# Kernel tuning notes

Measured on AMD Instinct MI355X. Metric: run time of the kernel, lower is better.

## Reference

```python
import jax, jax.numpy as jnp
import numpy as np

N = 200_000      # n_reflns
NIMG = 500       # n_images
DMETA = 24       # metadata features
WIDTH = 32       # mlp_width
HID = 64         # hidden_units = 2*width (FeedForward default)
DEPTH = 20       # mlp_depth
NPOST = 2        # Normal posterior: (loc, scale)
EPS = 1e-12
KLW = 0.01       # scaling_kl_weight


def setup_inputs() -> dict:
    key = jax.random.key(0)
    ks = jax.random.split(key, 10)
    metadata = jax.random.normal(ks[0], (N, DMETA), jnp.float32)
    iobs = jax.random.normal(ks[1], (N, 1), jnp.float32)
    sigiobs = jax.random.uniform(ks[2], (N, 1), jnp.float32)
    image_ids = jnp.sort(jax.random.randint(ks[3], (N,), 0, NIMG)).astype(jnp.int32)
    n_reflns_per_image = jnp.bincount(image_ids, length=NIMG).astype(jnp.int32)
    d_img = DMETA + 2  # concat(metadata, iobs, sigiobs)
    w_img_in = jax.random.normal(ks[4], (d_img, WIDTH), jnp.float32) / np.float32(np.sqrt(d_img))
    b_img_in = jnp.zeros((WIDTH,), jnp.float32)
    w_scale_in = jax.random.normal(ks[5], (DMETA, WIDTH), jnp.float32) / np.float32(np.sqrt(DMETA))
    b_scale_in = jnp.zeros((WIDTH,), jnp.float32)
    # shared residual FeedForward stack (share_weights=True): x + W2 @ relu(W1 @ x)
    mlp_w1 = jax.random.normal(ks[6], (DEPTH, WIDTH, HID), jnp.float32) / np.float32(np.sqrt(WIDTH))
    mlp_b1 = jnp.zeros((DEPTH, HID), jnp.float32)
    mlp_w2 = jax.random.normal(ks[7], (DEPTH, HID, WIDTH), jnp.float32) * np.float32(0.1 / np.sqrt(HID))
    mlp_b2 = jnp.zeros((DEPTH, WIDTH), jnp.float32)
    w_out = jax.random.normal(ks[8], (WIDTH, NPOST), jnp.float32) / np.float32(np.sqrt(WIDTH))
    b_out = jnp.zeros((NPOST,), jnp.float32)
    return {
        'metadata': metadata, 'iobs': iobs, 'sigiobs': sigiobs,
        'w_img_in': w_img_in, 'b_img_in': b_img_in,
        'w_scale_in': w_scale_in, 'b_scale_in': b_scale_in,
        'mlp_w1': mlp_w1, 'mlp_b1': mlp_b1, 'mlp_w2': mlp_w2, 'mlp_b2': mlp_b2,
        'w_out': w_out, 'b_out': b_out,
        'image_ids_in_this_batch': image_ids,
        'n_reflns_per_image': n_reflns_per_image,
        'mc_samples': 32,
    }


def _mlp(h, w1, b1, w2, b2):
    # depth residual FF blocks, weights stacked along leading DEPTH axis
    def block(h, ws):
        wa, ba, wb, bb = ws
        h = h + (jax.nn.relu(h @ wa + ba) @ wb + bb)
        return h, None
    h, _ = jax.lax.scan(block, h, (w1, b1, w2, b2))
    return h


def reference(metadata, iobs, sigiobs,
              w_img_in, b_img_in, w_scale_in, b_scale_in,
              mlp_w1, mlp_b1, mlp_w2, mlp_b2, w_out, b_out,
              image_ids_in_this_batch, n_reflns_per_image, mc_samples):
    image = jnp.concatenate([metadata, iobs, sigiobs], axis=-1)   # (N, DMETA+2)
    h = image @ w_img_in + b_img_in                               # (N, W)
    h = _mlp(h, mlp_w1, mlp_b1, mlp_w2, mlp_b2)
    nimg = n_reflns_per_image.shape[0]
    sums = jax.ops.segment_sum(h, image_ids_in_this_batch, num_segments=nimg)
    counts = jnp.maximum(n_reflns_per_image, 1).astype(h.dtype)[:, None]
    pooled = sums / counts                                        # (NIMG, W) image-average pool
    s = metadata @ w_scale_in + b_scale_in + pooled[image_ids_in_this_batch]
    s = _mlp(s, mlp_w1, mlp_b1, mlp_w2, mlp_b2)                   # shared weights
    params = s @ w_out + b_out                                    # (N, 2)
    loc = params[:, 0]
    scale = jax.nn.softplus(params[:, 1]) + EPS
    # rsample from Normal(loc, scale), mc_samples draws
    noise = jax.random.normal(jax.random.key(42), (mc_samples, loc.shape[0]), loc.dtype)
    z = loc + scale * noise                                       # (S, N)
    # MC KL estimate: mean_s[log q(z) - log p(z)], p = Laplace(0, 1)
    log_q = -0.5 * jnp.square(noise) - jnp.log(scale) - np.float32(0.5 * np.log(2.0 * np.pi))
    log_p = -jnp.abs(z) - np.float32(np.log(2.0))
    kl_div = KLW * jnp.mean(log_q - log_p, axis=0)                # (N,)
    return z.T, kl_div
```

## Files before the change

### kernel.cpp

```cpp
#include <hip/hip_runtime.h>
#include <stdint.h>

#define N_ROWS 200000
#define NIMG   500
#define DMETA  24
#define WIDTH  32
#define HID    64
#define DEPTH  20
#define MC     32
#define NSTR   18

typedef __attribute__((ext_vector_type(8))) short bf16x8;
typedef __attribute__((ext_vector_type(4))) float f32x4;

#define MFMA(a, b, acc) __builtin_amdgcn_mfma_f32_16x16x32_bf16((a), (b), (acc), 0, 0, 0)

#define OFF_W1H  64000
#define OFF_W1L  145920
#define OFF_W2H  227840
#define OFF_W2L  309760
#define OFF_WIH  391680
#define OFF_WIL  393728
#define OFF_WSH  395776
#define OFF_WSL  397824

__device__ __forceinline__ uint32_t rotl32(uint32_t x, int r) {
    return (x << r) | (x >> (32 - r));
}

__device__ __forceinline__ uint32_t tf_bits(uint32_t j) {
    const uint32_t ks1 = 42u, ks2 = 0x1BD11BDAu ^ 42u;
    uint32_t x0 = 0u, x1 = j + ks1;
#define R4(a,b,c,d) \
    x0 += x1; x1 = rotl32(x1,(a)); x1 ^= x0; \
    x0 += x1; x1 = rotl32(x1,(b)); x1 ^= x0; \
    x0 += x1; x1 = rotl32(x1,(c)); x1 ^= x0; \
    x0 += x1; x1 = rotl32(x1,(d)); x1 ^= x0;
    R4(13,15,26,6)  x0 += ks1; x1 += ks2 + 1u;
    R4(17,29,16,24) x0 += ks2; x1 += 0u + 2u;
    R4(13,15,26,6)                x1 += ks1 + 3u;
    R4(17,29,16,24) x0 += ks1; x1 += ks2 + 4u;
    R4(13,15,26,6)  x0 += ks2; x1 += 0u + 5u;
#undef R4
    return x0 ^ x1;
}

__device__ __forceinline__ float bits_to_normal(uint32_t b) {
    float f = __uint_as_float((b >> 9) | 0x3f800000u) - 1.0f;
    const float lo = -0.99999994f;
    float u = fmaxf(lo, f * 2.0f + lo);
    return 1.41421356f * erfinvf(u);
}

__device__ __forceinline__ void split1(float x, short& hi, short& lo) {
    uint32_t b = __float_as_uint(x);
    uint32_t a = b + 0x8000u;
    hi = (short)(a >> 16);
    float r = x - __uint_as_float(a & 0xFFFF0000u);
    lo = (short)(__float_as_uint(r) >> 16);
}

__device__ __forceinline__ void split8p(const float* x, bf16x8& hi, bf16x8& lo) {
    uint32_t hu[4], lu[4];
#pragma unroll
    for (int p = 0; p < 4; ++p) {
        uint32_t b0 = __float_as_uint(x[2 * p]);
        uint32_t b1 = __float_as_uint(x[2 * p + 1]);
        uint32_t a0 = b0 + 0x8000u, a1 = b1 + 0x8000u;
        hu[p] = __builtin_amdgcn_perm(a1, a0, 0x07060302u);
        float r0 = x[2 * p] - __uint_as_float(a0 & 0xFFFF0000u);
        float r1 = x[2 * p + 1] - __uint_as_float(a1 & 0xFFFF0000u);
        lu[p] = __builtin_amdgcn_perm(__float_as_uint(r1), __float_as_uint(r0), 0x07060302u);
    }
    __builtin_memcpy(&hi, hu, 16);
    __builtin_memcpy(&lo, lu, 16);
}

__device__ __forceinline__ void mlp20_x2(
    float* hC0, float* hC1, float* smw0, float* smw1,
    const short* __restrict__ w1fh, const short* __restrict__ w1fl,
    const short* __restrict__ w2fh, const short* __restrict__ w2fl,
    const float* __restrict__ b1, const float* __restrict__ b2,
    int lane, int q, int c) {
    float2* sm20 = (float2*)smw0;
    float2* sm21 = (float2*)smw1;
#pragma unroll 1
    for (int l = 0; l < DEPTH; ++l) {
#pragma unroll
        for (int t = 0; t < 2; ++t) {
            int bi = (16 * t + c) * 9 + 2 * q;
            sm20[bi]     = make_float2(hC0[t * 4 + 0], hC0[t * 4 + 1]);
            sm20[bi + 1] = make_float2(hC0[t * 4 + 2], hC0[t * 4 + 3]);
            sm21[bi]     = make_float2(hC1[t * 4 + 0], hC1[t * 4 + 1]);
            sm21[bi + 1] = make_float2(hC1[t * 4 + 2], hC1[t * 4 + 3]);
        }
        float a0[8], a1[8];
#pragma unroll
        for (int j = 0; j < 8; ++j) a0[j] = smw0[(q * 8 + j) * NSTR + c];
#pragma unroll
        for (int j = 0; j < 8; ++j) a1[j] = smw1[(q * 8 + j) * NSTR + c];
        bf16x8 ah0, al0, ah1, al1;
        split8p(a0, ah0, al0);
        split8p(a1, ah1, al1);
        float C1v0[16], C1v1[16];
#pragma unroll
        for (int t = 0; t < 4; ++t) {
            const int fi = (((l * 4 + t) << 9) + (lane << 3));
            bf16x8 bh = *(const bf16x8*)(w1fh + fi);
            bf16x8 bl = *(const bf16x8*)(w1fl + fi);
            float bb = b1[l * 64 + 16 * t + c];
            f32x4 acc = {0.f, 0.f, 0.f, 0.f};
            acc = MFMA(ah0, bh, acc); acc = MFMA(ah0, bl, acc); acc = MFMA(al0, bh, acc);
            f32x4 acd = {0.f, 0.f, 0.f, 0.f};
            acd = MFMA(ah1, bh, acd); acd = MFMA(ah1, bl, acd); acd = MFMA(al1, bh, acd);
#pragma unroll
            for (int r = 0; r < 4; ++r) {
                C1v0[t * 4 + r] = fmaxf(acc[r] + bb, 0.0f);
                C1v1[t * 4 + r] = fmaxf(acd[r] + bb, 0.0f);
            }
        }
#pragma unroll
        for (int t = 0; t < 4; ++t) {
            int bi = (16 * t + c) * 9 + 2 * q;
            sm20[bi]     = make_float2(C1v0[t * 4 + 0], C1v0[t * 4 + 1]);
            sm20[bi + 1] = make_float2(C1v0[t * 4 + 2], C1v0[t * 4 + 3]);
            sm21[bi]     = make_float2(C1v1[t * 4 + 0], C1v1[t * 4 + 1]);
            sm21[bi + 1] = make_float2(C1v1[t * 4 + 2], C1v1[t * 4 + 3]);
        }
        f32x4 acc0[2], acc1[2];
#pragma unroll
        for (int t2 = 0; t2 < 2; ++t2)
#pragma unroll
            for (int r = 0; r < 4; ++r) {
                acc0[t2][r] = hC0[t2 * 4 + r];
                acc1[t2][r] = hC1[t2 * 4 + r];
            }
#pragma unroll
        for (int kf = 0; kf < 2; ++kf) {
            float e0[8], e1[8];
#pragma unroll
            for (int j = 0; j < 8; ++j) e0[j] = smw0[(kf * 32 + q * 8 + j) * NSTR + c];
#pragma unroll
            for (int j = 0; j < 8; ++j) e1[j] = smw1[(kf * 32 + q * 8 + j) * NSTR + c];
            bf16x8 xh0, xl0, xh1, xl1;
            split8p(e0, xh0, xl0);
            split8p(e1, xh1, xl1);
#pragma unroll
            for (int t2 = 0; t2 < 2; ++t2) {
                const int fi = ((((l * 2 + kf) * 2 + t2) << 9) + (lane << 3));
                bf16x8 bh = *(const bf16x8*)(w2fh + fi);
                bf16x8 bl = *(const bf16x8*)(w2fl + fi);
                acc0[t2] = MFMA(xh0, bh, acc0[t2]);
                acc0[t2] = MFMA(xh0, bl, acc0[t2]);
                acc0[t2] = MFMA(xl0, bh, acc0[t2]);
                acc1[t2] = MFMA(xh1, bh, acc1[t2]);
                acc1[t2] = MFMA(xh1, bl, acc1[t2]);
                acc1[t2] = MFMA(xl1, bh, acc1[t2]);
            }
        }
#pragma unroll
        for (int t2 = 0; t2 < 2; ++t2) {
            float bb = b2[l * 32 + 16 * t2 + c];
#pragma unroll
            for (int r = 0; r < 4; ++r) {
                hC0[t2 * 4 + r] = acc0[t2][r] + bb;
                hC1[t2 * 4 + r] = acc1[t2][r] + bb;
            }
        }
    }
}

__device__ __forceinline__ void input_proj(
    const bf16x8& ah, const bf16x8& al, const short* __restrict__ wfh,
    const short* __restrict__ wfl, const float* __restrict__ bias,
    float* hC, int lane, int c) {
#pragma unroll
    for (int t = 0; t < 2; ++t) {
        bf16x8 bh = *(const bf16x8*)(wfh + ((t << 9) + (lane << 3)));
        bf16x8 bl = *(const bf16x8*)(wfl + ((t << 9) + (lane << 3)));
        f32x4 acc = {0.f, 0.f, 0.f, 0.f};
        acc = MFMA(ah, bh, acc); acc = MFMA(ah, bl, acc); acc = MFMA(al, bh, acc);
        float bb = bias[16 * t + c];
#pragma unroll
        for (int r = 0; r < 4; ++r) hC[t * 4 + r] = acc[r] + bb;
    }
}

__global__ __launch_bounds__(256) void prep_kernel(
    const float* __restrict__ w1, const float* __restrict__ w2,
    const float* __restrict__ wimg, const float* __restrict__ wsc,
    char* __restrict__ wsb) {
    int t = blockIdx.x * 256 + threadIdx.x;
    float* sums = (float*)wsb;
    if (t < 16000) { sums[t] = 0.0f; return; }
    t -= 16000;
    if (t < 40960) {
        int l = t >> 11, r = t & 2047, tt = r >> 9, r2 = r & 511;
        int lane = r2 >> 3, j = r2 & 7;
        int k = (lane >> 4) * 8 + j, n = 16 * tt + (lane & 15);
        short h, lo;
        split1(w1[l * 2048 + k * 64 + n], h, lo);
        ((short*)(wsb + OFF_W1H))[t] = h;
        ((short*)(wsb + OFF_W1L))[t] = lo;
        return;
    }
    t -= 40960;
    if (t < 40960) {
        int l = t >> 11, r = t & 2047, kf = r >> 10, r2 = r & 1023;
        int t2 = r2 >> 9, r3 = r2 & 511, lane = r3 >> 3, j = r3 & 7;
        int k = kf * 32 + (lane >> 4) * 8 + j, n = 16 * t2 + (lane & 15);
        short h, lo;
        split1(w2[l * 2048 + k * 32 + n], h, lo);
        ((short*)(wsb + OFF_W2H))[t] = h;
        ((short*)(wsb + OFF_W2L))[t] = lo;
        return;
    }
    t -= 40960;
    if (t < 1024) {
        int tt = t >> 9, r = t & 511, lane = r >> 3, j = r & 7;
        int k = (lane >> 4) * 8 + j, n = 16 * tt + (lane & 15);
        float v = (k < 26) ? wimg[k * 32 + n] : 0.0f;
        short h, lo;
        split1(v, h, lo);
        ((short*)(wsb + OFF_WIH))[t] = h;
        ((short*)(wsb + OFF_WIL))[t] = lo;
        return;
    }
    t -= 1024;
    if (t < 1024) {
        int tt = t >> 9, r = t & 511, lane = r >> 3, j = r & 7;
        int k = (lane >> 4) * 8 + j, n = 16 * tt + (lane & 15);
        float v = (k < 24) ? wsc[k * 32 + n] : 0.0f;
        short h, lo;
        split1(v, h, lo);
        ((short*)(wsb + OFF_WSH))[t] = h;
        ((short*)(wsb + OFF_WSL))[t] = lo;
        return;
    }
}

__device__ __forceinline__ void load_xfrag(
    const float* __restrict__ md, const float* __restrict__ iobs,
    const float* __restrict__ sig, int base, int q, int c,
    bf16x8& ah, bf16x8& al) {
    float xa[8];
    if (q < 3) {
        const f32x4* rp = (const f32x4*)(md + (size_t)(base + c) * DMETA + q * 8);
        f32x4 v0 = rp[0], v1 = rp[1];
#pragma unroll
        for (int j = 0; j < 4; ++j) { xa[j] = v0[j]; xa[4 + j] = v1[j]; }
    } else {
        xa[0] = iobs ? iobs[base + c] : 0.0f;
        xa[1] = sig ? sig[base + c] : 0.0f;
#pragma unroll
        for (int j = 2; j < 8; ++j) xa[j] = 0.0f;
    }
    split8p(xa, ah, al);
}

__global__ __launch_bounds__(128, 4) void pass_a(
    const float* __restrict__ md, const float* __restrict__ iobs,
    const float* __restrict__ sig, const float* __restrict__ bimg,
    const char* __restrict__ wsb, const float* __restrict__ b1,
    const float* __restrict__ b2, const int* __restrict__ ids,
    float* __restrict__ sums) {
    __shared__ float smat[2][2][64 * NSTR];
    int lane = threadIdx.x & 63, w = threadIdx.x >> 6;
    int q = lane >> 4, c = lane & 15;
    int i0 = (blockIdx.x * 2 + w) * 32;
    float* smw0 = &smat[w][0][0];
    float* smw1 = &smat[w][1][0];

    bf16x8 ah0, al0, ah1, al1;
    load_xfrag(md, iobs, sig, i0, q, c, ah0, al0);
    load_xfrag(md, iobs, sig, i0 + 16, q, c, ah1, al1);

    float hC0[8], hC1[8];
    input_proj(ah0, al0, (const short*)(wsb + OFF_WIH), (const short*)(wsb + OFF_WIL),
               bimg, hC0, lane, c);
    input_proj(ah1, al1, (const short*)(wsb + OFF_WIH), (const short*)(wsb + OFF_WIL),
               bimg, hC1, lane, c);

    mlp20_x2(hC0, hC1, smw0, smw1,
             (const short*)(wsb + OFF_W1H), (const short*)(wsb + OFF_W1L),
             (const short*)(wsb + OFF_W2H), (const short*)(wsb + OFF_W2L),
             b1, b2, lane, q, c);

#pragma unroll
    for (int tile = 0; tile < 2; ++tile) {
        const float* hC = tile ? hC1 : hC0;
        int tb = i0 + tile * 16;
        bool uni = (ids[tb] == ids[tb + 15]);
        if (uni) {
            int id = ids[tb];
#pragma unroll
            for (int t = 0; t < 2; ++t) {
                float s = (hC[t * 4 + 0] + hC[t * 4 + 1]) + (hC[t * 4 + 2] + hC[t * 4 + 3]);
                s += __shfl_xor(s, 16, 64);
                s += __shfl_xor(s, 32, 64);
                if (q == 0) atomicAdd(&sums[id * 32 + 16 * t + c], s);
            }
        } else {
            int idv[4];
#pragma unroll
            for (int r = 0; r < 4; ++r) idv[r] = ids[tb + q * 4 + r];
#pragma unroll
            for (int t = 0; t < 2; ++t)
#pragma unroll
                for (int r = 0; r < 4; ++r)
                    atomicAdd(&sums[idv[r] * 32 + 16 * t + c], hC[t * 4 + r]);
        }
    }
}

__global__ __launch_bounds__(256) void normalize_kernel(float* __restrict__ sums,
                                                        const int* __restrict__ cnts) {
    int t = blockIdx.x * 256 + threadIdx.x;
    if (t < NIMG * WIDTH) {
        int img = t >> 5;
        float cc = (float)max(cnts[img], 1);
        sums[t] = sums[t] / cc;
    }
}

__global__ __launch_bounds__(128, 4) void pass_b(
    const float* __restrict__ md, const float* __restrict__ bsc,
    const char* __restrict__ wsb, const float* __restrict__ b1,
    const float* __restrict__ b2, const float* __restrict__ wout,
    const float* __restrict__ bout, const int* __restrict__ ids,
    const float* __restrict__ pooled, float* __restrict__ out) {
    __shared__ float smat[2][2][64 * NSTR];
    __shared__ float sls[2][64];
    int lane = threadIdx.x & 63, w = threadIdx.x >> 6;
    int q = lane >> 4, c = lane & 15;
    int i0 = (blockIdx.x * 2 + w) * 32;
    float* smw0 = &smat[w][0][0];
    float* smw1 = &smat[w][1][0];

    bf16x8 ah0, al0, ah1, al1;
    load_xfrag(md, nullptr, nullptr, i0, q, c, ah0, al0);
    load_xfrag(md, nullptr, nullptr, i0 + 16, q, c, ah1, al1);

    float hC0[8], hC1[8];
    input_proj(ah0, al0, (const short*)(wsb + OFF_WSH), (const short*)(wsb + OFF_WSL),
               bsc, hC0, lane, c);
    input_proj(ah1, al1, (const short*)(wsb + OFF_WSH), (const short*)(wsb + OFF_WSL),
               bsc, hC1, lane, c);
#pragma unroll
    for (int tile = 0; tile < 2; ++tile) {
        float* hC = tile ? hC1 : hC0;
        int tb = i0 + tile * 16;
        int idv[4];
#pragma unroll
        for (int r = 0; r < 4; ++r) idv[r] = ids[tb + q * 4 + r];
#pragma unroll
        for (int t = 0; t < 2; ++t)
#pragma unroll
            for (int r = 0; r < 4; ++r)
                hC[t * 4 + r] += pooled[idv[r] * 32 + 16 * t + c];
    }

    mlp20_x2(hC0, hC1, smw0, smw1,
             (const short*)(wsb + OFF_W1H), (const short*)(wsb + OFF_W1L),
             (const short*)(wsb + OFF_W2H), (const short*)(wsb + OFF_W2L),
             b1, b2, lane, q, c);

    float wo0[2], wo1[2];
#pragma unroll
    for (int t = 0; t < 2; ++t) {
        float2 wv = ((const float2*)wout)[16 * t + c];
        wo0[t] = wv.x; wo1[t] = wv.y;
    }
#pragma unroll
    for (int tile = 0; tile < 2; ++tile) {
        const float* hC = tile ? hC1 : hC0;
        float p0r[4], p1r[4];
#pragma unroll
        for (int r = 0; r < 4; ++r) {
            p0r[r] = hC[r] * wo0[0] + hC[4 + r] * wo0[1];
            p1r[r] = hC[r] * wo1[0] + hC[4 + r] * wo1[1];
        }
#pragma unroll
        for (int m = 1; m < 16; m <<= 1) {
#pragma unroll
            for (int r = 0; r < 4; ++r) {
                p0r[r] += __shfl_xor(p0r[r], m, 64);
                p1r[r] += __shfl_xor(p1r[r], m, 64);
            }
        }
        if (c == 0) {
#pragma unroll
            for (int r = 0; r < 4; ++r) {
                float loc = p0r[r] + bout[0];
                float pb = p1r[r] + bout[1];
                float scale = fmaxf(pb, 0.0f) + log1pf(expf(-fabsf(pb))) + 1e-12f;
                sls[w][tile * 16 + q * 4 + r] = loc;
                sls[w][32 + tile * 16 + q * 4 + r] = scale;
            }
        }
    }

    int ro = lane & 31, half = lane >> 5;
    int row = i0 + ro;
    float L = sls[w][ro];
    float S = sls[w][32 + ro];
    float lsg = logf(S);
    float kp = 0.0f;
    float* zrow = out + (size_t)row * MC + half * 16;
#pragma unroll 4
    for (int s4 = 0; s4 < 4; ++s4) {
        f32x4 zv;
#pragma unroll
        for (int jj = 0; jj < 4; ++jj) {
            int t = half * 16 + s4 * 4 + jj;
            uint32_t j = (uint32_t)(t * N_ROWS) + (uint32_t)row;
            float n = bits_to_normal(tf_bits(j));
            float z = fmaf(S, n, L);
            zv[jj] = z;
            kp += fmaf(-0.5f, n * n, fabsf(z));
        }
        *(f32x4*)(zrow + s4 * 4) = zv;
    }
    kp += __shfl_xor(kp, 32, 64);
    if (half == 0) {
        out[(size_t)N_ROWS * MC + row] =
            0.01f * (kp * (1.0f / 32.0f) - lsg - 0.91893853320467274f + 0.69314718055994531f);
    }
}

extern "C" void kernel_launch(void* const* d_in, const int* in_sizes, int n_in,
                              void* d_out, int out_size, void* d_ws, size_t ws_size,
                              hipStream_t stream) {
    const float* md   = (const float*)d_in[0];
    const float* iobs = (const float*)d_in[1];
    const float* sig  = (const float*)d_in[2];
    const float* wimg = (const float*)d_in[3];
    const float* bimg = (const float*)d_in[4];
    const float* wsc  = (const float*)d_in[5];
    const float* bsc  = (const float*)d_in[6];
    const float* w1   = (const float*)d_in[7];
    const float* b1   = (const float*)d_in[8];
    const float* w2   = (const float*)d_in[9];
    const float* b2   = (const float*)d_in[10];
    const float* wout = (const float*)d_in[11];
    const float* bout = (const float*)d_in[12];
    const int* ids    = (const int*)d_in[13];
    const int* cnts   = (const int*)d_in[14];
    float* out = (float*)d_out;
    char* wsb = (char*)d_ws;
    float* sums = (float*)wsb;

    const int nblk = N_ROWS / 64;
    prep_kernel<<<391, 256, 0, stream>>>(w1, w2, wimg, wsc, wsb);
    pass_a<<<nblk, 128, 0, stream>>>(md, iobs, sig, bimg, wsb, b1, b2, ids, sums);
    normalize_kernel<<<(NIMG * WIDTH + 255) / 256, 256, 0, stream>>>(sums, cnts);
    pass_b<<<nblk, 128, 0, stream>>>(md, bsc, wsb, b1, b2, wout, bout, ids, sums, out);
}
```

Baseline: 395.4 us.

## Keep MLP activations in registers via transposed 16x16x16 MFMA layout

Rewrites the residual MLP so that weights become the A operand and activations the B operand of 16x16x16 bf16 MFMAs. The output layout of one layer then matches the input layout of the next, so the shared-memory round trip and the LDS re-read that transposed activations each layer are removed. Weight hi/lo fragments are interleaved into one 16-byte load per fragment. Pooling atomics, the pooled gather and the output head are adapted to the new row-per-column layout. The trade-off is twice as many smaller MFMA instructions and different register pressure.

```diff
diff --git a/kernel.cpp b/kernel.cpp
--- a/kernel.cpp
+++ b/kernel.cpp
@@ -8,21 +8,19 @@
 #define HID    64
 #define DEPTH  20
 #define MC     32
-#define NSTR   18
-
+
+typedef __attribute__((ext_vector_type(4))) short bf16x4;
 typedef __attribute__((ext_vector_type(8))) short bf16x8;
 typedef __attribute__((ext_vector_type(4))) float f32x4;
 
-#define MFMA(a, b, acc) __builtin_amdgcn_mfma_f32_16x16x32_bf16((a), (b), (acc), 0, 0, 0)
-
-#define OFF_W1H  64000
-#define OFF_W1L  145920
-#define OFF_W2H  227840
-#define OFF_W2L  309760
-#define OFF_WIH  391680
-#define OFF_WIL  393728
-#define OFF_WSH  395776
-#define OFF_WSL  397824
+__device__ __forceinline__ f32x4 MFMA16(bf16x4 a, bf16x4 b, f32x4 c) {
+    return __builtin_amdgcn_mfma_f32_16x16x16bf16_1k(a, b, c, 0, 0, 0);
+}
+
+#define OFF_W1 64000
+#define OFF_W2 227840
+#define OFF_WI 391680
+#define OFF_WS 395776
 
 __device__ __forceinline__ uint32_t rotl32(uint32_t x, int r) {
     return (x << r) | (x >> (32 - r));
@@ -64,9 +62,8 @@
     uint32_t hu[4], lu[4];
 #pragma unroll
     for (int p = 0; p < 4; ++p) {
-        uint32_t b0 = __float_as_uint(x[2 * p]);
-        uint32_t b1 = __float_as_uint(x[2 * p + 1]);
-        uint32_t a0 = b0 + 0x8000u, a1 = b1 + 0x8000u;
+        uint32_t a0 = __float_as_uint(x[2 * p]) + 0x8000u;
+        uint32_t a1 = __float_as_uint(x[2 * p + 1]) + 0x8000u;
         hu[p] = __builtin_amdgcn_perm(a1, a0, 0x07060302u);
         float r0 = x[2 * p] - __uint_as_float(a0 & 0xFFFF0000u);
         float r1 = x[2 * p + 1] - __uint_as_float(a1 & 0xFFFF0000u);
@@ -76,113 +73,131 @@
     __builtin_memcpy(&lo, lu, 16);
 }
 
-__device__ __forceinline__ void mlp20_x2(
-    float* hC0, float* hC1, float* smw0, float* smw1,
-    const short* __restrict__ w1fh, const short* __restrict__ w1fl,
-    const short* __restrict__ w2fh, const short* __restrict__ w2fl,
+__device__ __forceinline__ void split4p(const float* x, bf16x4& hi, bf16x4& lo) {
+    uint32_t hu[2], lu[2];
+#pragma unroll
+    for (int p = 0; p < 2; ++p) {
+        uint32_t a0 = __float_as_uint(x[2 * p]) + 0x8000u;
+        uint32_t a1 = __float_as_uint(x[2 * p + 1]) + 0x8000u;
+        hu[p] = __builtin_amdgcn_perm(a1, a0, 0x07060302u);
+        float r0 = x[2 * p] - __uint_as_float(a0 & 0xFFFF0000u);
+        float r1 = x[2 * p + 1] - __uint_as_float(a1 & 0xFFFF0000u);
+        lu[p] = __builtin_amdgcn_perm(__float_as_uint(r1), __float_as_uint(r0), 0x07060302u);
+    }
+    __builtin_memcpy(&hi, hu, 8);
+    __builtin_memcpy(&lo, lu, 8);
+}
+
+__device__ __forceinline__ bf16x4 vlo(bf16x8 v) { bf16x4 r = {v[0], v[1], v[2], v[3]}; return r; }
+__device__ __forceinline__ bf16x4 vhi(bf16x8 v) { bf16x4 r = {v[4], v[5], v[6], v[7]}; return r; }
+
+__device__ __forceinline__ void mlp20_reg(
+    float* hC0, float* hC1,
+    const short* __restrict__ w1f, const short* __restrict__ w2f,
     const float* __restrict__ b1, const float* __restrict__ b2,
-    int lane, int q, int c) {
-    float2* sm20 = (float2*)smw0;
-    float2* sm21 = (float2*)smw1;
+    int lane, int q) {
+    const int fo = lane * 8;
 #pragma unroll 1
     for (int l = 0; l < DEPTH; ++l) {
-#pragma unroll
-        for (int t = 0; t < 2; ++t) {
-            int bi = (16 * t + c) * 9 + 2 * q;
-            sm20[bi]     = make_float2(hC0[t * 4 + 0], hC0[t * 4 + 1]);
-            sm20[bi + 1] = make_float2(hC0[t * 4 + 2], hC0[t * 4 + 3]);
-            sm21[bi]     = make_float2(hC1[t * 4 + 0], hC1[t * 4 + 1]);
-            sm21[bi + 1] = make_float2(hC1[t * 4 + 2], hC1[t * 4 + 3]);
-        }
-        float a0[8], a1[8];
-#pragma unroll
-        for (int j = 0; j < 8; ++j) a0[j] = smw0[(q * 8 + j) * NSTR + c];
-#pragma unroll
-        for (int j = 0; j < 8; ++j) a1[j] = smw1[(q * 8 + j) * NSTR + c];
-        bf16x8 ah0, al0, ah1, al1;
-        split8p(a0, ah0, al0);
-        split8p(a1, ah1, al1);
-        float C1v0[16], C1v1[16];
-#pragma unroll
-        for (int t = 0; t < 4; ++t) {
-            const int fi = (((l * 4 + t) << 9) + (lane << 3));
-            bf16x8 bh = *(const bf16x8*)(w1fh + fi);
-            bf16x8 bl = *(const bf16x8*)(w1fl + fi);
-            float bb = b1[l * 64 + 16 * t + c];
-            f32x4 acc = {0.f, 0.f, 0.f, 0.f};
-            acc = MFMA(ah0, bh, acc); acc = MFMA(ah0, bl, acc); acc = MFMA(al0, bh, acc);
-            f32x4 acd = {0.f, 0.f, 0.f, 0.f};
-            acd = MFMA(ah1, bh, acd); acd = MFMA(ah1, bl, acd); acd = MFMA(al1, bh, acd);
+        bf16x8 s0h, s0l, s1h, s1l;
+        split8p(hC0, s0h, s0l);
+        split8p(hC1, s1h, s1l);
+        bf16x4 c0h[2] = {vlo(s0h), vhi(s0h)}, c0l[2] = {vlo(s0l), vhi(s0l)};
+        bf16x4 c1h[2] = {vlo(s1h), vhi(s1h)}, c1l[2] = {vlo(s1l), vhi(s1l)};
+        float Y0[16], Y1[16];
+        const short* wp1 = w1f + l * 4096;
+#pragma unroll
+        for (int Mt = 0; Mt < 4; ++Mt) {
+            f32x4 bb = *(const f32x4*)(b1 + l * 64 + 16 * Mt + 4 * q);
+            f32x4 a0 = {0.f, 0.f, 0.f, 0.f}, a1 = {0.f, 0.f, 0.f, 0.f};
+#pragma unroll
+            for (int Kc = 0; Kc < 2; ++Kc) {
+                bf16x8 wf = *(const bf16x8*)(wp1 + (Mt * 2 + Kc) * 512 + fo);
+                bf16x4 wh = vlo(wf), wl = vhi(wf);
+                a0 = MFMA16(wh, c0h[Kc], a0);
+                a0 = MFMA16(wh, c0l[Kc], a0);
+                a0 = MFMA16(wl, c0h[Kc], a0);
+                a1 = MFMA16(wh, c1h[Kc], a1);
+                a1 = MFMA16(wh, c1l[Kc], a1);
+                a1 = MFMA16(wl, c1h[Kc], a1);
+            }
 #pragma unroll
             for (int r = 0; r < 4; ++r) {
-                C1v0[t * 4 + r] = fmaxf(acc[r] + bb, 0.0f);
-                C1v1[t * 4 + r] = fmaxf(acd[r] + bb, 0.0f);
+                Y0[Mt * 4 + r] = fmaxf(a0[r] + bb[r], 0.0f);
+                Y1[Mt * 4 + r] = fmaxf(a1[r] + bb[r], 0.0f);
             }
         }
-#pragma unroll
-        for (int t = 0; t < 4; ++t) {
-            int bi = (16 * t + c) * 9 + 2 * q;
-            sm20[bi]     = make_float2(C1v0[t * 4 + 0], C1v0[t * 4 + 1]);
-            sm20[bi + 1] = make_float2(C1v0[t * 4 + 2], C1v0[t * 4 + 3]);
-            sm21[bi]     = make_float2(C1v1[t * 4 + 0], C1v1[t * 4 + 1]);
-            sm21[bi + 1] = make_float2(C1v1[t * 4 + 2], C1v1[t * 4 + 3]);
-        }
-        f32x4 acc0[2], acc1[2];
-#pragma unroll
-        for (int t2 = 0; t2 < 2; ++t2)
+        bf16x8 y0h0, y0l0, y0h1, y0l1, y1h0, y1l0, y1h1, y1l1;
+        split8p(Y0, y0h0, y0l0); split8p(Y0 + 8, y0h1, y0l1);
+        split8p(Y1, y1h0, y1l0); split8p(Y1 + 8, y1h1, y1l1);
+        bf16x4 yb0[4] = {vlo(y0h0), vhi(y0h0), vlo(y0h1), vhi(y0h1)};
+        bf16x4 ys0[4] = {vlo(y0l0), vhi(y0l0), vlo(y0l1), vhi(y0l1)};
+        bf16x4 yb1[4] = {vlo(y1h0), vhi(y1h0), vlo(y1h1), vhi(y1h1)};
+        bf16x4 ys1[4] = {vlo(y1l0), vhi(y1l0), vlo(y1l1), vhi(y1l1)};
+        const short* wp2 = w2f + l * 4096;
+#pragma unroll
+        for (int Mt2 = 0; Mt2 < 2; ++Mt2) {
+            f32x4 bb = *(const f32x4*)(b2 + l * 32 + 16 * Mt2 + 4 * q);
+            f32x4 a0, a1;
+#pragma unroll
+            for (int r = 0; r < 4; ++r) { a0[r] = hC0[Mt2 * 4 + r]; a1[r] = hC1[Mt2 * 4 + r]; }
+#pragma unroll
+            for (int Kc = 0; Kc < 4; ++Kc) {
+                bf16x8 wf = *(const bf16x8*)(wp2 + (Mt2 * 4 + Kc) * 512 + fo);
+                bf16x4 wh = vlo(wf), wl = vhi(wf);
+                a0 = MFMA16(wh, yb0[Kc], a0);
+                a0 = MFMA16(wh, ys0[Kc], a0);
+                a0 = MFMA16(wl, yb0[Kc], a0);
+                a1 = MFMA16(wh, yb1[Kc], a1);
+                a1 = MFMA16(wh, ys1[Kc], a1);
+                a1 = MFMA16(wl, yb1[Kc], a1);
+            }
 #pragma unroll
             for (int r = 0; r < 4; ++r) {
-                acc0[t2][r] = hC0[t2 * 4 + r];
-                acc1[t2][r] = hC1[t2 * 4 + r];
+                hC0[Mt2 * 4 + r] = a0[r] + bb[r];
+                hC1[Mt2 * 4 + r] = a1[r] + bb[r];
             }
-#pragma unroll
-        for (int kf = 0; kf < 2; ++kf) {
-            float e0[8], e1[8];
-#pragma unroll
-            for (int j = 0; j < 8; ++j) e0[j] = smw0[(kf * 32 + q * 8 + j) * NSTR + c];
-#pragma unroll
-            for (int j = 0; j < 8; ++j) e1[j] = smw1[(kf * 32 + q * 8 + j) * NSTR + c];
-            bf16x8 xh0, xl0, xh1, xl1;
-            split8p(e0, xh0, xl0);
-            split8p(e1, xh1, xl1);
-#pragma unroll
-            for (int t2 = 0; t2 < 2; ++t2) {
-                const int fi = ((((l * 2 + kf) * 2 + t2) << 9) + (lane << 3));
-                bf16x8 bh = *(const bf16x8*)(w2fh + fi);
-                bf16x8 bl = *(const bf16x8*)(w2fl + fi);
-                acc0[t2] = MFMA(xh0, bh, acc0[t2]);
-                acc0[t2] = MFMA(xh0, bl, acc0[t2]);
-                acc0[t2] = MFMA(xl0, bh, acc0[t2]);
-                acc1[t2] = MFMA(xh1, bh, acc1[t2]);
-                acc1[t2] = MFMA(xh1, bl, acc1[t2]);
-                acc1[t2] = MFMA(xl1, bh, acc1[t2]);
-            }
-        }
-#pragma unroll
-        for (int t2 = 0; t2 < 2; ++t2) {
-            float bb = b2[l * 32 + 16 * t2 + c];
-#pragma unroll
-            for (int r = 0; r < 4; ++r) {
-                hC0[t2 * 4 + r] = acc0[t2][r] + bb;
-                hC1[t2 * 4 + r] = acc1[t2][r] + bb;
-            }
-        }
-    }
-}
-
-__device__ __forceinline__ void input_proj(
-    const bf16x8& ah, const bf16x8& al, const short* __restrict__ wfh,
-    const short* __restrict__ wfl, const float* __restrict__ bias,
-    float* hC, int lane, int c) {
-#pragma unroll
-    for (int t = 0; t < 2; ++t) {
-        bf16x8 bh = *(const bf16x8*)(wfh + ((t << 9) + (lane << 3)));
-        bf16x8 bl = *(const bf16x8*)(wfl + ((t << 9) + (lane << 3)));
-        f32x4 acc = {0.f, 0.f, 0.f, 0.f};
-        acc = MFMA(ah, bh, acc); acc = MFMA(ah, bl, acc); acc = MFMA(al, bh, acc);
-        float bb = bias[16 * t + c];
-#pragma unroll
-        for (int r = 0; r < 4; ++r) hC[t * 4 + r] = acc[r] + bb;
+        }
+    }
+}
+
+__device__ __forceinline__ void load_xchunks(
+    const float* __restrict__ md, const float* __restrict__ iobs,
+    const float* __restrict__ sig, int row, int q,
+    bf16x4* bh, bf16x4* bl) {
+    f32x4 x0 = *(const f32x4*)(md + (size_t)row * DMETA + 4 * q);
+    float x0v[4] = {x0[0], x0[1], x0[2], x0[3]};
+    float x1v[4] = {0.f, 0.f, 0.f, 0.f};
+    if (q < 2) {
+        f32x4 tv = *(const f32x4*)(md + (size_t)row * DMETA + 16 + 4 * q);
+        x1v[0] = tv[0]; x1v[1] = tv[1]; x1v[2] = tv[2]; x1v[3] = tv[3];
+    } else if (q == 2) {
+        x1v[0] = iobs ? iobs[row] : 0.f;
+        x1v[1] = sig ? sig[row] : 0.f;
+    }
+    split4p(x0v, bh[0], bl[0]);
+    split4p(x1v, bh[1], bl[1]);
+}
+
+__device__ __forceinline__ void in_proj(
+    const bf16x4* bh, const bf16x4* bl,
+    const short* __restrict__ wf, const float* __restrict__ bias,
+    float* hC, int lane, int q) {
+    const int fo = lane * 8;
+#pragma unroll
+    for (int Mt = 0; Mt < 2; ++Mt) {
+        f32x4 bb = *(const f32x4*)(bias + 16 * Mt + 4 * q);
+        f32x4 a = {0.f, 0.f, 0.f, 0.f};
+#pragma unroll
+        for (int Kc = 0; Kc < 2; ++Kc) {
+            bf16x8 wf8 = *(const bf16x8*)(wf + (Mt * 2 + Kc) * 512 + fo);
+            bf16x4 wh = vlo(wf8), wl = vhi(wf8);
+            a = MFMA16(wh, bh[Kc], a);
+            a = MFMA16(wh, bl[Kc], a);
+            a = MFMA16(wl, bh[Kc], a);
+        }
+#pragma unroll
+        for (int r = 0; r < 4; ++r) hC[Mt * 4 + r] = a[r] + bb[r];
     }
 }
 
@@ -195,67 +210,48 @@
     if (t < 16000) { sums[t] = 0.0f; return; }
     t -= 16000;
     if (t < 40960) {
-        int l = t >> 11, r = t & 2047, tt = r >> 9, r2 = r & 511;
-        int lane = r2 >> 3, j = r2 & 7;
-        int k = (lane >> 4) * 8 + j, n = 16 * tt + (lane & 15);
-        short h, lo;
-        split1(w1[l * 2048 + k * 64 + n], h, lo);
-        ((short*)(wsb + OFF_W1H))[t] = h;
-        ((short*)(wsb + OFF_W1L))[t] = lo;
+        int l = t >> 11, rem = t & 2047, frag = rem >> 8, vs = rem & 255;
+        int lane = vs >> 2, j = vs & 3, q = lane >> 4, c = lane & 15;
+        int Mt = frag >> 1, Kc = frag & 1;
+        int k = 16 * Kc + 4 * q + j, n = 16 * Mt + c;
+        short h, lo; split1(w1[l * 2048 + k * 64 + n], h, lo);
+        short* dst = (short*)(wsb + OFF_W1) + l * 4096 + frag * 512 + lane * 8;
+        dst[j] = h; dst[4 + j] = lo;
         return;
     }
     t -= 40960;
     if (t < 40960) {
-        int l = t >> 11, r = t & 2047, kf = r >> 10, r2 = r & 1023;
-        int t2 = r2 >> 9, r3 = r2 & 511, lane = r3 >> 3, j = r3 & 7;
-        int k = kf * 32 + (lane >> 4) * 8 + j, n = 16 * t2 + (lane & 15);
-        short h, lo;
-        split1(w2[l * 2048 + k * 32 + n], h, lo);
-        ((short*)(wsb + OFF_W2H))[t] = h;
-        ((short*)(wsb + OFF_W2L))[t] = lo;
+        int l = t >> 11, rem = t & 2047, frag = rem >> 8, vs = rem & 255;
+        int lane = vs >> 2, j = vs & 3, q = lane >> 4, c = lane & 15;
+        int Mt2 = frag >> 2, Kc = frag & 3;
+        int k = 16 * Kc + 4 * q + j, n = 16 * Mt2 + c;
+        short h, lo; split1(w2[l * 2048 + k * 32 + n], h, lo);
+        short* dst = (short*)(wsb + OFF_W2) + l * 4096 + frag * 512 + lane * 8;
+        dst[j] = h; dst[4 + j] = lo;
         return;
     }
     t -= 40960;
     if (t < 1024) {
-        int tt = t >> 9, r = t & 511, lane = r >> 3, j = r & 7;
-        int k = (lane >> 4) * 8 + j, n = 16 * tt + (lane & 15);
+        int frag = t >> 8, vs = t & 255, lane = vs >> 2, j = vs & 3;
+        int q = lane >> 4, c = lane & 15, Mt = frag >> 1, Kc = frag & 1;
+        int k = 16 * Kc + 4 * q + j, n = 16 * Mt + c;
         float v = (k < 26) ? wimg[k * 32 + n] : 0.0f;
-        short h, lo;
-        split1(v, h, lo);
-        ((short*)(wsb + OFF_WIH))[t] = h;
-        ((short*)(wsb + OFF_WIL))[t] = lo;
+        short h, lo; split1(v, h, lo);
+        short* dst = (short*)(wsb + OFF_WI) + frag * 512 + lane * 8;
+        dst[j] = h; dst[4 + j] = lo;
         return;
     }
     t -= 1024;
     if (t < 1024) {
-        int tt = t >> 9, r = t & 511, lane = r >> 3, j = r & 7;
-        int k = (lane >> 4) * 8 + j, n = 16 * tt + (lane & 15);
+        int frag = t >> 8, vs = t & 255, lane = vs >> 2, j = vs & 3;
+        int q = lane >> 4, c = lane & 15, Mt = frag >> 1, Kc = frag & 1;
+        int k = 16 * Kc + 4 * q + j, n = 16 * Mt + c;
         float v = (k < 24) ? wsc[k * 32 + n] : 0.0f;
-        short h, lo;
-        split1(v, h, lo);
-        ((short*)(wsb + OFF_WSH))[t] = h;
-        ((short*)(wsb + OFF_WSL))[t] = lo;
+        short h, lo; split1(v, h, lo);
+        short* dst = (short*)(wsb + OFF_WS) + frag * 512 + lane * 8;
+        dst[j] = h; dst[4 + j] = lo;
         return;
     }
-}
-
-__device__ __forceinline__ void load_xfrag(
-    const float* __restrict__ md, const float* __restrict__ iobs,
-    const float* __restrict__ sig, int base, int q, int c,
-    bf16x8& ah, bf16x8& al) {
-    float xa[8];
-    if (q < 3) {
-        const f32x4* rp = (const f32x4*)(md + (size_t)(base + c) * DMETA + q * 8);
-        f32x4 v0 = rp[0], v1 = rp[1];
-#pragma unroll
-        for (int j = 0; j < 4; ++j) { xa[j] = v0[j]; xa[4 + j] = v1[j]; }
-    } else {
-        xa[0] = iobs ? iobs[base + c] : 0.0f;
-        xa[1] = sig ? sig[base + c] : 0.0f;
-#pragma unroll
-        for (int j = 2; j < 8; ++j) xa[j] = 0.0f;
-    }
-    split8p(xa, ah, al);
 }
 
 __global__ __launch_bounds__(128, 4) void pass_a(
@@ -264,51 +260,48 @@
     const char* __restrict__ wsb, const float* __restrict__ b1,
     const float* __restrict__ b2, const int* __restrict__ ids,
     float* __restrict__ sums) {
-    __shared__ float smat[2][2][64 * NSTR];
     int lane = threadIdx.x & 63, w = threadIdx.x >> 6;
     int q = lane >> 4, c = lane & 15;
     int i0 = (blockIdx.x * 2 + w) * 32;
-    float* smw0 = &smat[w][0][0];
-    float* smw1 = &smat[w][1][0];
-
-    bf16x8 ah0, al0, ah1, al1;
-    load_xfrag(md, iobs, sig, i0, q, c, ah0, al0);
-    load_xfrag(md, iobs, sig, i0 + 16, q, c, ah1, al1);
+
+    bf16x4 bh0[2], bl0[2], bh1[2], bl1[2];
+    load_xchunks(md, iobs, sig, i0 + c, q, bh0, bl0);
+    load_xchunks(md, iobs, sig, i0 + 16 + c, q, bh1, bl1);
 
     float hC0[8], hC1[8];
-    input_proj(ah0, al0, (const short*)(wsb + OFF_WIH), (const short*)(wsb + OFF_WIL),
-               bimg, hC0, lane, c);
-    input_proj(ah1, al1, (const short*)(wsb + OFF_WIH), (const short*)(wsb + OFF_WIL),
-               bimg, hC1, lane, c);
-
-    mlp20_x2(hC0, hC1, smw0, smw1,
-             (const short*)(wsb + OFF_W1H), (const short*)(wsb + OFF_W1L),
-             (const short*)(wsb + OFF_W2H), (const short*)(wsb + OFF_W2L),
-             b1, b2, lane, q, c);
+    in_proj(bh0, bl0, (const short*)(wsb + OFF_WI), bimg, hC0, lane, q);
+    in_proj(bh1, bl1, (const short*)(wsb + OFF_WI), bimg, hC1, lane, q);
+
+    mlp20_reg(hC0, hC1, (const short*)(wsb + OFF_W1), (const short*)(wsb + OFF_W2),
+              b1, b2, lane, q);
 
 #pragma unroll
     for (int tile = 0; tile < 2; ++tile) {
-        const float* hC = tile ? hC1 : hC0;
+        float* hC = tile ? hC1 : hC0;
         int tb = i0 + tile * 16;
-        bool uni = (ids[tb] == ids[tb + 15]);
-        if (uni) {
-            int id = ids[tb];
-#pragma unroll
-            for (int t = 0; t < 2; ++t) {
-                float s = (hC[t * 4 + 0] + hC[t * 4 + 1]) + (hC[t * 4 + 2] + hC[t * 4 + 3]);
-                s += __shfl_xor(s, 16, 64);
-                s += __shfl_xor(s, 32, 64);
-                if (q == 0) atomicAdd(&sums[id * 32 + 16 * t + c], s);
+        if (ids[tb] == ids[tb + 15]) {
+            float v[8];
+#pragma unroll
+            for (int r = 0; r < 8; ++r) v[r] = hC[r];
+#pragma unroll
+            for (int m = 1; m < 16; m <<= 1)
+#pragma unroll
+                for (int r = 0; r < 8; ++r) v[r] += __shfl_xor(v[r], m, 64);
+            if (c == 0) {
+                int id = ids[tb];
+#pragma unroll
+                for (int t = 0; t < 2; ++t)
+#pragma unroll
+                    for (int r = 0; r < 4; ++r)
+                        atomicAdd(&sums[id * 32 + 16 * t + 4 * q + r], v[t * 4 + r]);
             }
         } else {
-            int idv[4];
-#pragma unroll
-            for (int r = 0; r < 4; ++r) idv[r] = ids[tb + q * 4 + r];
+            int id = ids[tb + c];
 #pragma unroll
             for (int t = 0; t < 2; ++t)
 #pragma unroll
                 for (int r = 0; r < 4; ++r)
-                    atomicAdd(&sums[idv[r] * 32 + 16 * t + c], hC[t * 4 + r]);
+                    atomicAdd(&sums[id * 32 + 16 * t + 4 * q + r], hC[t * 4 + r]);
         }
     }
 }
@@ -329,82 +322,62 @@
     const float* __restrict__ b2, const float* __restrict__ wout,
     const float* __restrict__ bout, const int* __restrict__ ids,
     const float* __restrict__ pooled, float* __restrict__ out) {
-    __shared__ float smat[2][2][64 * NSTR];
-    __shared__ float sls[2][64];
     int lane = threadIdx.x & 63, w = threadIdx.x >> 6;
     int q = lane >> 4, c = lane & 15;
     int i0 = (blockIdx.x * 2 + w) * 32;
-    float* smw0 = &smat[w][0][0];
-    float* smw1 = &smat[w][1][0];
-
-    bf16x8 ah0, al0, ah1, al1;
-    load_xfrag(md, nullptr, nullptr, i0, q, c, ah0, al0);
-    load_xfrag(md, nullptr, nullptr, i0 + 16, q, c, ah1, al1);
+
+    bf16x4 bh0[2], bl0[2], bh1[2], bl1[2];
+    load_xchunks(md, nullptr, nullptr, i0 + c, q, bh0, bl0);
+    load_xchunks(md, nullptr, nullptr, i0 + 16 + c, q, bh1, bl1);
 
     float hC0[8], hC1[8];
-    input_proj(ah0, al0, (const short*)(wsb + OFF_WSH), (const short*)(wsb + OFF_WSL),
-               bsc, hC0, lane, c);
-    input_proj(ah1, al1, (const short*)(wsb + OFF_WSH), (const short*)(wsb + OFF_WSL),
-               bsc, hC1, lane, c);
+    in_proj(bh0, bl0, (const short*)(wsb + OFF_WS), bsc, hC0, lane, q);
+    in_proj(bh1, bl1, (const short*)(wsb + OFF_WS), bsc, hC1, lane, q);
+
 #pragma unroll
     for (int tile = 0; tile < 2; ++tile) {
         float* hC = tile ? hC1 : hC0;
-        int tb = i0 + tile * 16;
-        int idv[4];
-#pragma unroll
-        for (int r = 0; r < 4; ++r) idv[r] = ids[tb + q * 4 + r];
-#pragma unroll
-        for (int t = 0; t < 2; ++t)
-#pragma unroll
-            for (int r = 0; r < 4; ++r)
-                hC[t * 4 + r] += pooled[idv[r] * 32 + 16 * t + c];
-    }
-
-    mlp20_x2(hC0, hC1, smw0, smw1,
-             (const short*)(wsb + OFF_W1H), (const short*)(wsb + OFF_W1L),
-             (const short*)(wsb + OFF_W2H), (const short*)(wsb + OFF_W2L),
-             b1, b2, lane, q, c);
-
-    float wo0[2], wo1[2];
-#pragma unroll
-    for (int t = 0; t < 2; ++t) {
-        float2 wv = ((const float2*)wout)[16 * t + c];
-        wo0[t] = wv.x; wo1[t] = wv.y;
-    }
+        int idv = ids[i0 + tile * 16 + c];
+#pragma unroll
+        for (int t = 0; t < 2; ++t) {
+            f32x4 pv = *(const f32x4*)(pooled + idv * 32 + 16 * t + 4 * q);
+#pragma unroll
+            for (int r = 0; r < 4; ++r) hC[t * 4 + r] += pv[r];
+        }
+    }
+
+    mlp20_reg(hC0, hC1, (const short*)(wsb + OFF_W1), (const short*)(wsb + OFF_W2),
+              b1, b2, lane, q);
+
+    float loc_t[2], sc_t[2];
 #pragma unroll
     for (int tile = 0; tile < 2; ++tile) {
         const float* hC = tile ? hC1 : hC0;
-        float p0r[4], p1r[4];
-#pragma unroll
-        for (int r = 0; r < 4; ++r) {
-            p0r[r] = hC[r] * wo0[0] + hC[4 + r] * wo0[1];
-            p1r[r] = hC[r] * wo1[0] + hC[4 + r] * wo1[1];
-        }
-#pragma unroll
-        for (int m = 1; m < 16; m <<= 1) {
-#pragma unroll
-            for (int r = 0; r < 4; ++r) {
-                p0r[r] += __shfl_xor(p0r[r], m, 64);
-                p1r[r] += __shfl_xor(p1r[r], m, 64);
-            }
-        }
-        if (c == 0) {
-#pragma unroll
-            for (int r = 0; r < 4; ++r) {
-                float loc = p0r[r] + bout[0];
-                float pb = p1r[r] + bout[1];
-                float scale = fmaxf(pb, 0.0f) + log1pf(expf(-fabsf(pb))) + 1e-12f;
-                sls[w][tile * 16 + q * 4 + r] = loc;
-                sls[w][32 + tile * 16 + q * 4 + r] = scale;
-            }
-        }
-    }
-
-    int ro = lane & 31, half = lane >> 5;
+        float p0 = 0.f, p1 = 0.f;
+#pragma unroll
+        for (int t = 0; t < 2; ++t) {
+            f32x4 wA = *(const f32x4*)(wout + (16 * t + 4 * q) * 2);
+            f32x4 wB = *(const f32x4*)(wout + (16 * t + 4 * q) * 2 + 4);
+            p0 += hC[t * 4 + 0] * wA[0] + hC[t * 4 + 1] * wA[2]
+                + hC[t * 4 + 2] * wB[0] + hC[t * 4 + 3] * wB[2];
+            p1 += hC[t * 4 + 0] * wA[1] + hC[t * 4 + 1] * wA[3]
+                + hC[t * 4 + 2] * wB[1] + hC[t * 4 + 3] * wB[3];
+        }
+        p0 += __shfl_xor(p0, 16, 64); p0 += __shfl_xor(p0, 32, 64);
+        p1 += __shfl_xor(p1, 16, 64); p1 += __shfl_xor(p1, 32, 64);
+        float loc = p0 + bout[0];
+        float pb = p1 + bout[1];
+        loc_t[tile] = loc;
+        sc_t[tile] = fmaxf(pb, 0.0f) + log1pf(expf(-fabsf(pb))) + 1e-12f;
+    }
+
+    int ro = lane & 31, half = lane >> 5, cs = ro & 15;
+    float L0 = __shfl(loc_t[0], cs, 64), L1 = __shfl(loc_t[1], cs, 64);
+    float S0 = __shfl(sc_t[0], cs, 64),  S1 = __shfl(sc_t[1], cs, 64);
+    float L = (ro < 16) ? L0 : L1;
+    float S = (ro < 16) ? S0 : S1;
+    float lsg = logf(S);
     int row = i0 + ro;
-    float L = sls[w][ro];
-    float S = sls[w][32 + ro];
-    float lsg = logf(S);
     float kp = 0.0f;
     float* zrow = out + (size_t)row * MC + half * 16;
 #pragma unroll 4
```

Result: no change. 397.7 us (+0.6%).
